# Kernel optimization log

Hardware: AMD Instinct MI355X
Metric: run time of the kernel (lower is better)

## Reference

```python
import jax, jax.numpy as jnp
import numpy as np
from jax import lax

B, NP = 4, 8192          # events, points per event (equal-sized batches)
RATIO, R, K = 0.25, 0.2, 64
MP = int(NP * RATIO)     # sampled centers per event
D_IN = 32
BIG = 1e10


def _fps_one(pos):
    # Farthest point sampling (deterministic start at index 0). pos: [NP,3] -> [MP] int32
    d = jnp.sum((pos - pos[0]) ** 2, axis=-1)
    sel = jnp.zeros((MP,), jnp.int32)

    def body(i, carry):
        sel, d = carry
        nxt = jnp.argmax(d).astype(jnp.int32)
        sel = sel.at[i].set(nxt)
        d = jnp.minimum(d, jnp.sum((pos - pos[nxt]) ** 2, axis=-1))
        return sel, d

    sel, _ = lax.fori_loop(1, MP, body, (sel, d))
    return sel


def _ball_query_one(centers, pos):
    # centers: [MP,3], pos: [NP,3] -> neighbor idx [MP,K] int32, validity mask [MP,K]
    d2 = jnp.sum((centers[:, None, :] - pos[None, :, :]) ** 2, axis=-1)  # [MP,NP]
    d2m = jnp.where(d2 <= R * R, d2, BIG)
    neg, idx = lax.top_k(-d2m, K)          # K nearest within radius (deterministic)
    mask = (-neg) <= R * R
    return idx.astype(jnp.int32), mask


def reference(x, pos, batch, W1, b1, W2, b2, W3, b3):
    xb = x.reshape(B, NP, D_IN)
    pb = pos.reshape(B, NP, 3)

    sel = jax.vmap(_fps_one)(pb)                                   # [B,MP]
    centers = jnp.take_along_axis(pb, sel[..., None], axis=1)      # [B,MP,3]
    idx, mask = jax.vmap(_ball_query_one)(centers, pb)             # [B,MP,K]

    gather = jax.vmap(lambda a, i: a[i])
    pos_j = gather(pb, idx)                                        # [B,MP,K,3]
    x_j = gather(xb, idx)                                          # [B,MP,K,D_IN]

    rel = pos_j - centers[:, :, None, :]
    h = jnp.concatenate([x_j, rel], axis=-1)                       # [B,MP,K,D_IN+3]
    h = jax.nn.relu(h @ W1 + b1)
    h = jax.nn.relu(h @ W2 + b2)
    h = jax.nn.relu(h @ W3 + b3)                                   # [B,MP,K,128]

    h = jnp.where(mask[..., None], h, -BIG)
    x_out = jnp.max(h, axis=2).reshape(B * MP, -1)                 # max aggregation
    pos_out = centers.reshape(B * MP, 3)
    batch_out = jnp.repeat(jnp.arange(B, dtype=jnp.int32), MP)
    return x_out, pos_out, batch_out


def setup_inputs() -> dict:
    key = jax.random.key(0)
    ks = jax.random.split(key, 8)
    x = jax.random.normal(ks[0], (B * NP, D_IN), jnp.float32)
    pos = jax.random.uniform(ks[1], (B * NP, 3), jnp.float32)
    batch = (jnp.arange(B * NP) // NP).astype(jnp.int64)
    W1 = jax.random.normal(ks[2], (D_IN + 3, 64), jnp.float32) * 0.05
    b1 = jnp.zeros((64,), jnp.float32)
    W2 = jax.random.normal(ks[3], (64, 64), jnp.float32) * 0.05
    b2 = jnp.zeros((64,), jnp.float32)
    W3 = jax.random.normal(ks[4], (64, 128), jnp.float32) * 0.05
    b3 = jnp.zeros((128,), jnp.float32)
    return {"x": x, "pos": pos, "batch": batch, "W1": W1, "b1": b1,
            "W2": W2, "b2": b2, "W3": W3, "b3": b3}
```

## Files before the change

### kernel.cpp

```cpp
#include <hip/hip_runtime.h>


#define BATCH 4
#define NP 8192
#define MP 2048
#define KNN 64
#define DIN 32

#define DPP_FMAX(v, ctrl)                                                     \
  {                                                                           \
    int _t = __builtin_amdgcn_update_dpp(__float_as_int(v),                   \
                                         __float_as_int(v), (ctrl), 0xF,      \
                                         0xF, false);                         \
    (v) = fmaxf((v), __int_as_float(_t));                                     \
  }

#define DPP_MINU(v, ctrl)                                                     \
  {                                                                           \
    unsigned _t = (unsigned)__builtin_amdgcn_update_dpp((int)(v), (int)(v),   \
                                                        (ctrl), 0xF, 0xF,    \
                                                        false);               \
    (v) = ((v) < _t) ? (v) : _t;                                              \
  }

typedef float v2f __attribute__((ext_vector_type(2)));

__global__ __launch_bounds__(1024) void fps_k(const float* __restrict__ pos,
                                              const float* __restrict__ x,
                                              const float* __restrict__ W1,
                                              const float* __restrict__ W2,
                                              const float* __restrict__ W3,
                                              float* __restrict__ pout,
                                              float* __restrict__ bout,
                                              float* __restrict__ P1,
                                              float* __restrict__ W2T,
                                              float* __restrict__ W3T)
{
  const int bid = blockIdx.x;
  const int tid = threadIdx.x;

  if (bid >= BATCH) {
    if (bid < BATCH + 2048) {
      const int j = (bid - BATCH) * 16 + (tid >> 6);
      const int c = tid & 63;
      const float* __restrict__ xr = x + (size_t)j * DIN;
      float acc = 0.f;
#pragma unroll
      for (int k = 0; k < DIN; k++) acc += xr[k] * W1[k * 64 + c];
      P1[(size_t)j * 64 + c] = acc;
    } else {
#pragma unroll
      for (int it = 0; it < 12; it++) {
        const int e = it * 1024 + tid;
        if (e < 64 * 64) {
          const int c = e >> 6, k = e & 63;
          W2T[e] = W2[k * 64 + c];
        } else {
          const int e2 = e - 64 * 64;
          const int c = e2 >> 6, k = e2 & 63;
          W3T[e2] = W3[k * 128 + c];
        }
      }
    }
    return;
  }

  const int b = bid;
  const int lane = tid & 63, wid = tid >> 6;
  const float* __restrict__ pb = pos + (size_t)b * NP * 3;
  const int base = tid * 8;

  bout[b * MP + tid] = (float)b;
  bout[b * MP + 1024 + tid] = (float)b;

  __shared__ __align__(16) float ptab[NP * 3];
  __shared__ unsigned long long slt[2][16];

  float t[24];
  const float4* __restrict__ pv = (const float4*)(pb + (size_t)tid * 24);
#pragma unroll
  for (int q = 0; q < 6; q++) *(float4*)&t[q * 4] = pv[q];
#pragma unroll
  for (int q = 0; q < 6; q++) *(float4*)&ptab[tid * 24 + q * 4] = *(float4*)&t[q * 4];

  v2f px[4], py[4], pz[4], d[4];
#pragma unroll
  for (int j = 0; j < 4; j++) {
    px[j].x = t[6 * j + 0]; py[j].x = t[6 * j + 1]; pz[j].x = t[6 * j + 2];
    px[j].y = t[6 * j + 3]; py[j].y = t[6 * j + 4]; pz[j].y = t[6 * j + 5];
  }

  const float c0x = pb[0], c0y = pb[1], c0z = pb[2];
  if (tid == 0) {
    pout[(size_t)b * MP * 3 + 0] = c0x;
    pout[(size_t)b * MP * 3 + 1] = c0y;
    pout[(size_t)b * MP * 3 + 2] = c0z;
  }

  float bv = -1.f;
  {
    v2f cx = {c0x, c0x}, cy = {c0y, c0y}, cz = {c0z, c0z};
#pragma unroll
    for (int j = 0; j < 4; j++) {
      v2f dx = px[j] - cx, dy = py[j] - cy, dz = pz[j] - cz;
      v2f nd = dx * dx + dy * dy + dz * dz;
      d[j] = nd;
      bv = fmaxf(bv, fmaxf(nd.x, nd.y));
    }
  }

  for (int i = 1; i < MP; i++) {
    float v = bv;
    DPP_FMAX(v, 0x111);
    DPP_FMAX(v, 0x112);
    DPP_FMAX(v, 0x114);
    DPP_FMAX(v, 0x118);
    DPP_FMAX(v, 0x142);
    DPP_FMAX(v, 0x143);
    const float wmax =
        __int_as_float(__builtin_amdgcn_readlane(__float_as_int(v), 63));

    const unsigned long long m = __ballot(bv == wmax);
    const int src = (int)__builtin_ctzll(m);
    const int p = i & 1;
    if (lane == src) {
      int ks = 7;
#pragma unroll
      for (int k = 6; k >= 0; k--) {
        float dv = (k & 1) ? d[k >> 1].y : d[k >> 1].x;
        if (dv == wmax) ks = k;
      }
      slt[p][wid] = ((unsigned long long)__float_as_uint(wmax) << 32)
                    | (unsigned)(base + ks);
    }
    __syncthreads();

    const unsigned long long kv = slt[p][lane & 15];
    const float v2 = __uint_as_float((unsigned)(kv >> 32));
    float v2r = v2;
    DPP_FMAX(v2r, 0x111);
    DPP_FMAX(v2r, 0x112);
    DPP_FMAX(v2r, 0x114);
    DPP_FMAX(v2r, 0x118);
    const float mv =
        __int_as_float(__builtin_amdgcn_readlane(__float_as_int(v2r), 15));
    const unsigned long long m2 = __ballot(v2 == mv);
    const int mw = (int)__builtin_ctzll(m2);
    const int js = __builtin_amdgcn_readlane((int)(unsigned)kv, mw);
    const float ncx = ptab[js * 3 + 0];
    const float ncy = ptab[js * 3 + 1];
    const float ncz = ptab[js * 3 + 2];

    if (tid == 0) {
      pout[((size_t)b * MP + i) * 3 + 0] = ncx;
      pout[((size_t)b * MP + i) * 3 + 1] = ncy;
      pout[((size_t)b * MP + i) * 3 + 2] = ncz;
    }

    const v2f cx = {ncx, ncx}, cy = {ncy, ncy}, cz = {ncz, ncz};
    bv = -1.f;
#pragma unroll
    for (int j = 0; j < 4; j++) {
      v2f dx = px[j] - cx, dy = py[j] - cy, dz = pz[j] - cz;
      v2f nd = dx * dx + dy * dy + dz * dz;
      v2f dn;
      dn.x = fminf(d[j].x, nd.x);
      dn.y = fminf(d[j].y, nd.y);
      d[j] = dn;
      bv = fmaxf(bv, fmaxf(dn.x, dn.y));
    }
  }
}

__global__ __launch_bounds__(64) void bqmlp_k(const float* __restrict__ pos,
    const float* __restrict__ P1, const float* __restrict__ W1,
    const float* __restrict__ b1, const float* __restrict__ W2T,
    const float* __restrict__ b2, const float* __restrict__ W3T,
    const float* __restrict__ b3, const float* __restrict__ pout,
    float* __restrict__ xout)
{
  __shared__ __align__(16) float smem[64 * 68];
  unsigned long long* __restrict__ cand = (unsigned long long*)smem;

  const int wg = blockIdx.x;
  const int lane = threadIdx.x;
  const int b = wg >> 11;
  const float* __restrict__ pb = pos + (size_t)b * NP * 3;
  const float cx = pout[(size_t)wg * 3 + 0];
  const float cy = pout[(size_t)wg * 3 + 1];
  const float cz = pout[(size_t)wg * 3 + 2];
  const float R2 = (float)(0.2 * 0.2);

  int cnt = 0;
  for (int basej = 0; basej < NP; basej += 64) {
    const int j = basej + lane;
    float dx = pb[j * 3 + 0] - cx;
    float dy = pb[j * 3 + 1] - cy;
    float dz = pb[j * 3 + 2] - cz;
    float d2 = dx * dx + dy * dy + dz * dz;
    bool in = (d2 <= R2);
    unsigned long long mb = __ballot(in);
    int pre = (int)__popcll(mb & ((1ull << lane) - 1ull));
    int slot = cnt + pre;
    if (in && slot < 1024)
      cand[slot] = ((unsigned long long)__float_as_uint(d2) << 32) | (unsigned int)j;
    cnt += (int)__popcll(mb);
  }
  if (cnt > 1024) cnt = 1024;

  unsigned long long last = 0;
  int myout = -1;
  for (int r = 0; r < KNN; r++) {
    unsigned long long v = ~0ull;
    for (int s = lane; s < cnt; s += 64) {
      const unsigned long long c = cand[s];
      if (c >= last && c < v) v = c;
    }
    const unsigned hi = (unsigned)(v >> 32);
    unsigned h = hi;
    DPP_MINU(h, 0x111);
    DPP_MINU(h, 0x112);
    DPP_MINU(h, 0x114);
    DPP_MINU(h, 0x118);
    DPP_MINU(h, 0x142);
    DPP_MINU(h, 0x143);
    const unsigned mhi = (unsigned)__builtin_amdgcn_readlane((int)h, 63);
    const unsigned lo = (hi == mhi) ? (unsigned)v : 0xffffffffu;
    unsigned l2 = lo;
    DPP_MINU(l2, 0x111);
    DPP_MINU(l2, 0x112);
    DPP_MINU(l2, 0x114);
    DPP_MINU(l2, 0x118);
    DPP_MINU(l2, 0x142);
    DPP_MINU(l2, 0x143);
    const unsigned mlo = (unsigned)__builtin_amdgcn_readlane((int)l2, 63);

    if (lane == r) myout = (mhi == 0xffffffffu) ? -1 : (int)mlo;
    last = (mhi == 0xffffffffu)
               ? ~0ull
               : ((((unsigned long long)mhi << 32) | mlo) + 1ull);
  }

  __syncthreads();

  const int idx = myout;
  const bool valid = idx >= 0;
  const int j = valid ? idx : 0;
  const float* __restrict__ pj = pos + ((size_t)b * NP + j) * 3;
  const float rx = pj[0] - cx, ry = pj[1] - cy, rz = pj[2] - cz;
  const float* __restrict__ p1r =
      (const float*)__builtin_assume_aligned(P1 + ((size_t)b * NP + j) * 64, 16);

  float h1[64];
#pragma unroll
  for (int k = 0; k < 64; k++) {
    float v = p1r[k] + rx * W1[32 * 64 + k] + ry * W1[33 * 64 + k]
                     + rz * W1[34 * 64 + k] + b1[k];
    h1[k] = fmaxf(v, 0.f);
  }

  for (int c4 = 0; c4 < 16; c4++) {
    float a0 = b2[c4 * 4 + 0], a1 = b2[c4 * 4 + 1];
    float a2 = b2[c4 * 4 + 2], a3 = b2[c4 * 4 + 3];
    const float* __restrict__ w0 = W2T + (c4 * 4 + 0) * 64;
    const float* __restrict__ w1 = W2T + (c4 * 4 + 1) * 64;
    const float* __restrict__ w2 = W2T + (c4 * 4 + 2) * 64;
    const float* __restrict__ w3 = W2T + (c4 * 4 + 3) * 64;
#pragma unroll
    for (int k = 0; k < 64; k++) {
      a0 += h1[k] * w0[k]; a1 += h1[k] * w1[k];
      a2 += h1[k] * w2[k]; a3 += h1[k] * w3[k];
    }
    float4 q;
    q.x = fmaxf(a0, 0.f); q.y = fmaxf(a1, 0.f);
    q.z = fmaxf(a2, 0.f); q.w = fmaxf(a3, 0.f);
    *(float4*)&smem[lane * 68 + c4 * 4] = q;
  }

  float4 keep = make_float4(0.f, 0.f, 0.f, 0.f);
  const float* __restrict__ h2p = &smem[lane * 68];
  for (int c4 = 0; c4 < 32; c4++) {
    float a0 = b3[c4 * 4 + 0], a1 = b3[c4 * 4 + 1];
    float a2 = b3[c4 * 4 + 2], a3 = b3[c4 * 4 + 3];
    const float* __restrict__ w0 = W3T + (c4 * 4 + 0) * 64;
    const float* __restrict__ w1 = W3T + (c4 * 4 + 1) * 64;
    const float* __restrict__ w2 = W3T + (c4 * 4 + 2) * 64;
    const float* __restrict__ w3 = W3T + (c4 * 4 + 3) * 64;
#pragma unroll
    for (int k4 = 0; k4 < 16; k4++) {
      float4 h = *(const float4*)&h2p[k4 * 4];
      a0 += h.x * w0[k4 * 4 + 0]; a0 += h.y * w0[k4 * 4 + 1];
      a0 += h.z * w0[k4 * 4 + 2]; a0 += h.w * w0[k4 * 4 + 3];
      a1 += h.x * w1[k4 * 4 + 0]; a1 += h.y * w1[k4 * 4 + 1];
      a1 += h.z * w1[k4 * 4 + 2]; a1 += h.w * w1[k4 * 4 + 3];
      a2 += h.x * w2[k4 * 4 + 0]; a2 += h.y * w2[k4 * 4 + 1];
      a2 += h.z * w2[k4 * 4 + 2]; a2 += h.w * w2[k4 * 4 + 3];
      a3 += h.x * w3[k4 * 4 + 0]; a3 += h.y * w3[k4 * 4 + 1];
      a3 += h.z * w3[k4 * 4 + 2]; a3 += h.w * w3[k4 * 4 + 3];
    }
    a0 = valid ? fmaxf(a0, 0.f) : 0.f;
    a1 = valid ? fmaxf(a1, 0.f) : 0.f;
    a2 = valid ? fmaxf(a2, 0.f) : 0.f;
    a3 = valid ? fmaxf(a3, 0.f) : 0.f;
#pragma unroll
    for (int off = 1; off < 64; off <<= 1) {
      a0 = fmaxf(a0, __shfl_xor(a0, off));
      a1 = fmaxf(a1, __shfl_xor(a1, off));
      a2 = fmaxf(a2, __shfl_xor(a2, off));
      a3 = fmaxf(a3, __shfl_xor(a3, off));
    }
    if (lane == c4) { keep.x = a0; keep.y = a1; keep.z = a2; keep.w = a3; }
  }
  if (lane < 32)
    *(float4*)&xout[(size_t)wg * 128 + lane * 4] = keep;
}

extern "C" void kernel_launch(void* const* d_in, const int* in_sizes, int n_in,
                              void* d_out, int out_size, void* d_ws, size_t ws_size,
                              hipStream_t stream)
{
  const float* x   = (const float*)d_in[0];
  const float* pos = (const float*)d_in[1];
  const float* W1 = (const float*)d_in[3];
  const float* b1 = (const float*)d_in[4];
  const float* W2 = (const float*)d_in[5];
  const float* b2 = (const float*)d_in[6];
  const float* W3 = (const float*)d_in[7];
  const float* b3 = (const float*)d_in[8];

  float* out  = (float*)d_out;
  float* xout = out;
  float* pout = out + 8192 * 128;
  float* bout = out + 8192 * 128 + 8192 * 3;

  char* ws = (char*)d_ws;
  float* P1  = (float*)ws;
  float* W2T = (float*)(ws + 8388608);
  float* W3T = (float*)(ws + 8404992);

  fps_k<<<dim3(BATCH + 2048 + 1), dim3(1024), 0, stream>>>(
      pos, x, W1, W2, W3, pout, bout, P1, W2T, W3T);
  bqmlp_k<<<dim3(BATCH * MP), dim3(64), 0, stream>>>(pos, P1, W1, b1, W2T, b2,
                                                     W3T, b3, pout, xout);
}
```

Before: 2.625 ms.

## Keep MLP hidden layer in registers and use DPP wave-max reductions

```diff
diff --git a/kernel.cpp b/kernel.cpp
--- a/kernel.cpp
+++ b/kernel.cpp
@@ -21,6 +21,16 @@
                                                         (ctrl), 0xF, 0xF,    \
                                                         false);               \
     (v) = ((v) < _t) ? (v) : _t;                                              \
+  }
+
+#define DPP_WAVEMAX6(v)                                                       \
+  {                                                                           \
+    DPP_FMAX(v, 0x111);                                                       \
+    DPP_FMAX(v, 0x112);                                                       \
+    DPP_FMAX(v, 0x114);                                                       \
+    DPP_FMAX(v, 0x118);                                                       \
+    DPP_FMAX(v, 0x142);                                                       \
+    DPP_FMAX(v, 0x143);                                                       \
   }
 
 typedef float v2f __attribute__((ext_vector_type(2)));
@@ -111,12 +121,7 @@
 
   for (int i = 1; i < MP; i++) {
     float v = bv;
-    DPP_FMAX(v, 0x111);
-    DPP_FMAX(v, 0x112);
-    DPP_FMAX(v, 0x114);
-    DPP_FMAX(v, 0x118);
-    DPP_FMAX(v, 0x142);
-    DPP_FMAX(v, 0x143);
+    DPP_WAVEMAX6(v);
     const float wmax =
         __int_as_float(__builtin_amdgcn_readlane(__float_as_int(v), 63));
 
@@ -179,8 +184,7 @@
     const float* __restrict__ b3, const float* __restrict__ pout,
     float* __restrict__ xout)
 {
-  __shared__ __align__(16) float smem[64 * 68];
-  unsigned long long* __restrict__ cand = (unsigned long long*)smem;
+  __shared__ unsigned long long cand[1024];
 
   const int wg = blockIdx.x;
   const int lane = threadIdx.x;
@@ -241,8 +245,6 @@
                : ((((unsigned long long)mhi << 32) | mlo) + 1ull);
   }
 
-  __syncthreads();
-
   const int idx = myout;
   const bool valid = idx >= 0;
   const int j = valid ? idx : 0;
@@ -259,57 +261,52 @@
     h1[k] = fmaxf(v, 0.f);
   }
 
-  for (int c4 = 0; c4 < 16; c4++) {
-    float a0 = b2[c4 * 4 + 0], a1 = b2[c4 * 4 + 1];
-    float a2 = b2[c4 * 4 + 2], a3 = b2[c4 * 4 + 3];
-    const float* __restrict__ w0 = W2T + (c4 * 4 + 0) * 64;
-    const float* __restrict__ w1 = W2T + (c4 * 4 + 1) * 64;
-    const float* __restrict__ w2 = W2T + (c4 * 4 + 2) * 64;
-    const float* __restrict__ w3 = W2T + (c4 * 4 + 3) * 64;
+  float h2[64];
+#pragma unroll
+  for (int c = 0; c < 64; c++) {
+    float a = b2[c];
+    const float* __restrict__ w = W2T + c * 64;
+#pragma unroll
+    for (int k = 0; k < 64; k++) a += h1[k] * w[k];
+    h2[c] = fmaxf(a, 0.f);
+  }
+
+  float4 keep = make_float4(0.f, 0.f, 0.f, 0.f);
+  for (int pass = 0; pass < 4; pass++) {
+    const float* __restrict__ wp = W3T + (size_t)(pass * 32) * 64;
+    const float* __restrict__ bp = b3 + pass * 32;
+    float acc[32];
+#pragma unroll
+    for (int g = 0; g < 32; g++) acc[g] = bp[g];
 #pragma unroll
     for (int k = 0; k < 64; k++) {
-      a0 += h1[k] * w0[k]; a1 += h1[k] * w1[k];
-      a2 += h1[k] * w2[k]; a3 += h1[k] * w3[k];
-    }
-    float4 q;
-    q.x = fmaxf(a0, 0.f); q.y = fmaxf(a1, 0.f);
-    q.z = fmaxf(a2, 0.f); q.w = fmaxf(a3, 0.f);
-    *(float4*)&smem[lane * 68 + c4 * 4] = q;
-  }
-
-  float4 keep = make_float4(0.f, 0.f, 0.f, 0.f);
-  const float* __restrict__ h2p = &smem[lane * 68];
-  for (int c4 = 0; c4 < 32; c4++) {
-    float a0 = b3[c4 * 4 + 0], a1 = b3[c4 * 4 + 1];
-    float a2 = b3[c4 * 4 + 2], a3 = b3[c4 * 4 + 3];
-    const float* __restrict__ w0 = W3T + (c4 * 4 + 0) * 64;
-    const float* __restrict__ w1 = W3T + (c4 * 4 + 1) * 64;
-    const float* __restrict__ w2 = W3T + (c4 * 4 + 2) * 64;
-    const float* __restrict__ w3 = W3T + (c4 * 4 + 3) * 64;
-#pragma unroll
-    for (int k4 = 0; k4 < 16; k4++) {
-      float4 h = *(const float4*)&h2p[k4 * 4];
-      a0 += h.x * w0[k4 * 4 + 0]; a0 += h.y * w0[k4 * 4 + 1];
-      a0 += h.z * w0[k4 * 4 + 2]; a0 += h.w * w0[k4 * 4 + 3];
-      a1 += h.x * w1[k4 * 4 + 0]; a1 += h.y * w1[k4 * 4 + 1];
-      a1 += h.z * w1[k4 * 4 + 2]; a1 += h.w * w1[k4 * 4 + 3];
-      a2 += h.x * w2[k4 * 4 + 0]; a2 += h.y * w2[k4 * 4 + 1];
-      a2 += h.z * w2[k4 * 4 + 2]; a2 += h.w * w2[k4 * 4 + 3];
-      a3 += h.x * w3[k4 * 4 + 0]; a3 += h.y * w3[k4 * 4 + 1];
-      a3 += h.z * w3[k4 * 4 + 2]; a3 += h.w * w3[k4 * 4 + 3];
-    }
-    a0 = valid ? fmaxf(a0, 0.f) : 0.f;
-    a1 = valid ? fmaxf(a1, 0.f) : 0.f;
-    a2 = valid ? fmaxf(a2, 0.f) : 0.f;
-    a3 = valid ? fmaxf(a3, 0.f) : 0.f;
-#pragma unroll
-    for (int off = 1; off < 64; off <<= 1) {
-      a0 = fmaxf(a0, __shfl_xor(a0, off));
-      a1 = fmaxf(a1, __shfl_xor(a1, off));
-      a2 = fmaxf(a2, __shfl_xor(a2, off));
-      a3 = fmaxf(a3, __shfl_xor(a3, off));
-    }
-    if (lane == c4) { keep.x = a0; keep.y = a1; keep.z = a2; keep.w = a3; }
+      const float hk = h2[k];
+#pragma unroll
+      for (int g = 0; g < 32; g++) acc[g] += hk * wp[g * 64 + k];
+    }
+#pragma unroll
+    for (int g4 = 0; g4 < 8; g4++) {
+      float a0 = valid ? fmaxf(acc[g4 * 4 + 0], 0.f) : 0.f;
+      float a1 = valid ? fmaxf(acc[g4 * 4 + 1], 0.f) : 0.f;
+      float a2 = valid ? fmaxf(acc[g4 * 4 + 2], 0.f) : 0.f;
+      float a3 = valid ? fmaxf(acc[g4 * 4 + 3], 0.f) : 0.f;
+      DPP_WAVEMAX6(a0);
+      DPP_WAVEMAX6(a1);
+      DPP_WAVEMAX6(a2);
+      DPP_WAVEMAX6(a3);
+      const float m0 =
+          __int_as_float(__builtin_amdgcn_readlane(__float_as_int(a0), 63));
+      const float m1 =
+          __int_as_float(__builtin_amdgcn_readlane(__float_as_int(a1), 63));
+      const float m2 =
+          __int_as_float(__builtin_amdgcn_readlane(__float_as_int(a2), 63));
+      const float m3 =
+          __int_as_float(__builtin_amdgcn_readlane(__float_as_int(a3), 63));
+      const int cch = pass * 8 + g4;
+      if (lane == cch) {
+        keep.x = m0; keep.y = m1; keep.z = m2; keep.w = m3;
+      }
+    }
   }
   if (lane < 32)
     *(float4*)&xout[(size_t)wg * 128 + lane * 4] = keep;
```

Result: faster. 2.475 ms (-5.7%).
